# Performance work log

Measured on AMD Instinct MI355X. Metric: run time of the kernel, lower is better.

The kernel has to match this reference:

```python
import jax, jax.numpy as jnp
import numpy as np

B, S, D, H, HD, R = 1, 3072, 2048, 16, 128, 16
ALPHA = 16.0
EPS = 1e-6


def _rope_freqs():
    # standard RoPE angles, interleave-duplicated so freqs[..., 0::2] gives the
    # per-pair cos values exactly as the torch module slices them
    inv = 1.0 / (10000.0 ** (np.arange(0, HD, 2, dtype=np.float32) / HD))  # [HD/2]
    ang = np.arange(S, dtype=np.float32)[:, None] * inv[None, :]           # [S, HD/2]
    cos = np.repeat(np.cos(ang), 2, axis=-1).reshape(1, S, 1, HD)
    sin = np.repeat(np.sin(ang), 2, axis=-1).reshape(1, S, 1, HD)
    return jnp.asarray(cos), jnp.asarray(sin)


def setup_inputs() -> dict:
    key = jax.random.key(0)
    ks = jax.random.split(key, 18)
    n = jax.random.normal
    WS = 0.02  # weight init scale
    freqs_cos, freqs_sin = _rope_freqs()
    return {
        "hidden_states": n(ks[0], (B, S, D), jnp.float32),
        "wq": n(ks[1], (D, D), jnp.float32) * WS,
        "bq": n(ks[2], (D,), jnp.float32) * WS,
        "wk": n(ks[3], (D, D), jnp.float32) * WS,
        "bk": n(ks[4], (D,), jnp.float32) * WS,
        "wv": n(ks[5], (D, D), jnp.float32) * WS,
        "bv": n(ks[6], (D,), jnp.float32) * WS,
        "wo": n(ks[7], (D, D), jnp.float32) * WS,
        "bo": n(ks[8], (D,), jnp.float32) * WS,
        "lq_down": n(ks[9], (R, D), jnp.float32) / R,
        "lq_up": n(ks[10], (D, R), jnp.float32) * WS,
        "lk_down": n(ks[11], (R, D), jnp.float32) / R,
        "lk_up": n(ks[12], (D, R), jnp.float32) * WS,
        "lv_down": n(ks[13], (R, D), jnp.float32) / R,
        "lv_up": n(ks[14], (D, R), jnp.float32) * WS,
        "lo_down": n(ks[15], (R, D), jnp.float32) / R,
        "lo_up": n(ks[16], (D, R), jnp.float32) * WS,
        "norm_q_w": jnp.ones((D,), jnp.float32),
        "norm_k_w": jnp.ones((D,), jnp.float32),
        "freqs_cos": freqs_cos,
        "freqs_sin": freqs_sin,
    }


def _lora(x, w_down, w_up, scale):
    return (x @ w_down.T) @ w_up.T * scale


def _rmsnorm(x, w):
    return x * jax.lax.rsqrt(jnp.mean(x * x, axis=-1, keepdims=True) + EPS) * w


def _apply_rotary(x, freqs_cos, freqs_sin):
    # x: [B,S,H,HD]; freqs: [1,S,1,HD]
    x1, x2 = x[..., 0::2], x[..., 1::2]
    c = freqs_cos[..., 0::2]
    s = freqs_sin[..., 1::2]
    even = x1 * c - x2 * s
    odd = x1 * s + x2 * c
    return jnp.stack([even, odd], axis=-1).reshape(x.shape)


def reference(hidden_states, wq, bq, wk, bk, wv, bv, wo, bo,
              lq_down, lq_up, lk_down, lk_up, lv_down, lv_up, lo_down, lo_up,
              norm_q_w, norm_k_w, freqs_cos, freqs_sin):
    scale = ALPHA / R
    x = hidden_states
    # qkv projections + LoRA adds (self-attention: encoder_hidden_states = hidden_states)
    q = x @ wq.T + bq + _lora(x, lq_down, lq_up, scale)
    k = x @ wk.T + bk + _lora(x, lk_down, lk_up, scale)
    v = x @ wv.T + bv + _lora(x, lv_down, lv_up, scale)
    # RMSNorm over full d_model, then split heads
    q = _rmsnorm(q, norm_q_w).reshape(B, S, H, HD)
    k = _rmsnorm(k, norm_k_w).reshape(B, S, H, HD)
    v = v.reshape(B, S, H, HD)
    # custom strided rotary embedding
    q = _apply_rotary(q, freqs_cos, freqs_sin)
    k = _apply_rotary(k, freqs_cos, freqs_sin)
    # SDPA (non-causal, no mask)
    scores = jnp.einsum('bihd,bjhd->bhij', q, k) / jnp.sqrt(jnp.float32(HD))
    attn = jax.nn.softmax(scores, axis=-1)
    o = jnp.einsum('bhij,bjhd->bihd', attn, v).reshape(B, S, D)
    # output projection + LoRA
    out = o @ wo.T + bo + _lora(o, lo_down, lo_up, scale)
    return out
```

## Files before the change

### kernel.cpp

```cpp
#include <hip/hip_runtime.h>
#include <stdint.h>

#define S_LEN 3072
#define DIM   2048
#define NH    16
#define HDIM  128
#define RANK  16
#define EPS_F 1e-6f
#define LORA_SCALE 1.0f
#define QK_SCALE 0.08838834764831845f
#define SM_MAX 24.0f

typedef unsigned short u16;
typedef __attribute__((ext_vector_type(8))) short short8;
typedef __attribute__((ext_vector_type(4))) float f32x4;
typedef __attribute__((ext_vector_type(4))) unsigned short u16x4;
typedef __attribute__((ext_vector_type(8))) unsigned short u16x8;
typedef __attribute__((ext_vector_type(2))) unsigned short u16x2;
typedef __attribute__((ext_vector_type(4))) float float4a;

__device__ __forceinline__ u16 f2b(float f) {
  uint32_t u = __builtin_bit_cast(uint32_t, f);
  u += 0x7fffu + ((u >> 16) & 1u);
  return (u16)(u >> 16);
}
__device__ __forceinline__ float b2f(u16 b) {
  uint32_t u = ((uint32_t)b) << 16;
  return __builtin_bit_cast(float, u);
}

__device__ __forceinline__ void g2l16(const void* g, void* l) {
  __builtin_amdgcn_global_load_lds(
      (__attribute__((address_space(1))) unsigned int*)g,
      (__attribute__((address_space(3))) unsigned int*)l, 16, 0, 0);
}

__global__ __launch_bounds__(256) void convf2b(const float* __restrict__ in,
                                               u16* __restrict__ out) {
  int i = (blockIdx.x * 256 + threadIdx.x) * 4;
  float4a v = *(const float4a*)(in + i);
  u16x4 o = { f2b(v[0]), f2b(v[1]), f2b(v[2]), f2b(v[3]) };
  *(u16x4*)(out + i) = o;
}

__global__ __launch_bounds__(256) void fold_lora(const float* __restrict__ W,
                                                 const float* __restrict__ lu,
                                                 const float* __restrict__ ld,
                                                 u16* __restrict__ out) {
  __shared__ float lds_ld[16][136];
  __shared__ float lds_lu[64][17];
  const int tid = threadIdx.x;
  const int k0 = blockIdx.x * 128, n0 = blockIdx.y * 64;
  {
    int idx = tid * 8, r = idx >> 7, c = idx & 127;
    const float* src = ld + r * DIM + k0 + c;
#pragma unroll
    for (int e = 0; e < 8; ++e) lds_ld[r][c + e] = src[e];
  }
  {
    int idx = tid * 4, n = idx >> 4, r4 = idx & 15;
    const float* src = lu + (size_t)(n0 + n) * RANK + r4;
#pragma unroll
    for (int e = 0; e < 4; ++e) lds_lu[n][r4 + e] = src[e];
  }
  __syncthreads();
  const int n = tid >> 2;
  const int kg = (tid & 3) * 32;
  float luv[RANK];
#pragma unroll
  for (int r = 0; r < RANK; ++r) luv[r] = lds_lu[n][r];
  const float* wrow = W + (size_t)(n0 + n) * DIM + k0 + kg;
  u16* orow = out + (size_t)(n0 + n) * DIM + k0 + kg;
#pragma unroll
  for (int j = 0; j < 8; ++j) {
    float4a acc = *(const float4a*)(wrow + j * 4);
#pragma unroll
    for (int r = 0; r < RANK; ++r) {
      float4a lv = *(const float4a*)&lds_ld[r][kg + j * 4];
      acc += LORA_SCALE * luv[r] * lv;
    }
    u16x4 o = { f2b(acc[0]), f2b(acc[1]), f2b(acc[2]), f2b(acc[3]) };
    *(u16x4*)(orow + j * 4) = o;
  }
}

__global__ __launch_bounds__(256, 2) void gemm_fused(
    const u16* __restrict__ A, const u16* __restrict__ B,
    const float* __restrict__ b0, const float* __restrict__ b1,
    const float* __restrict__ b2, u16* __restrict__ c0, u16* __restrict__ c1,
    u16* __restrict__ c2, float* __restrict__ Cf) {
  __shared__ __attribute__((aligned(16))) u16 As[128 * 64];
  __shared__ __attribute__((aligned(16))) u16 Bs[128 * 64];
  const int tid = threadIdx.x;
  const int wave = tid >> 6, lane = tid & 63;
  const int quad = lane >> 4, l15 = lane & 15;
  const int m0 = blockIdx.x * 128, n0 = blockIdx.y * 128;
  const int mat = n0 >> 11;
  const float* bias = (mat == 0) ? b0 : (mat == 1 ? b1 : b2);
  u16* Cb = (mat == 0) ? c0 : (mat == 1 ? c1 : c2);
  const int wr = wave >> 1, wc = wave & 1;
  f32x4 acc[4][4] = {};
  for (int kt = 0; kt < DIM / 64; ++kt) {
    __syncthreads();
#pragma unroll
    for (int i = 0; i < 4; ++i) {
      int chunk = i * 256 + wave * 64 + lane;
      int row = chunk >> 3, c8 = chunk & 7;
      g2l16(A + (size_t)(m0 + row) * DIM + kt * 64 + c8 * 8,
            As + (i * 256 + wave * 64) * 8);
      g2l16(B + (size_t)(n0 + row) * DIM + kt * 64 + c8 * 8,
            Bs + (i * 256 + wave * 64) * 8);
    }
    __syncthreads();
#pragma unroll
    for (int kc = 0; kc < 2; ++kc) {
      short8 af[4], bf[4];
#pragma unroll
      for (int tm = 0; tm < 4; ++tm)
        af[tm] = *(const short8*)(As + (wr * 64 + tm * 16 + l15) * 64 +
                                  kc * 32 + quad * 8);
#pragma unroll
      for (int tn = 0; tn < 4; ++tn)
        bf[tn] = *(const short8*)(Bs + (wc * 64 + tn * 16 + l15) * 64 +
                                  kc * 32 + quad * 8);
#pragma unroll
      for (int tm = 0; tm < 4; ++tm)
#pragma unroll
        for (int tn = 0; tn < 4; ++tn)
          acc[tm][tn] = __builtin_amdgcn_mfma_f32_16x16x32_bf16(
              af[tm], bf[tn], acc[tm][tn], 0, 0, 0);
    }
  }
#pragma unroll
  for (int tn = 0; tn < 4; ++tn) {
    int col = n0 + wc * 64 + tn * 16 + l15;
    int colL = col & (DIM - 1);
    float bcol = bias[colL];
#pragma unroll
    for (int tm = 0; tm < 4; ++tm) {
#pragma unroll
      for (int r = 0; r < 4; ++r) {
        int row = m0 + wr * 64 + tm * 16 + quad * 4 + r;
        float val = acc[tm][tn][r] + bcol;
        if (Cf) Cf[(size_t)row * DIM + colL] = val;
        else Cb[(size_t)row * DIM + colL] = f2b(val);
      }
    }
  }
}

__global__ __launch_bounds__(256) void rms_rope(
    u16* __restrict__ q, u16* __restrict__ k,
    const float* __restrict__ nqw, const float* __restrict__ nkw,
    const float* __restrict__ fc, const float* __restrict__ fs) {
  const int s = blockIdx.x, tid = threadIdx.x;
  const int wave = tid >> 6, lane = tid & 63;
  float qv[8], kv[8];
  float sq = 0.f, sk = 0.f;
#pragma unroll
  for (int i = 0; i < 4; ++i) {
    int p = i * 256 + tid;
    u16x2 qa = *(const u16x2*)(q + (size_t)s * DIM + 2 * p);
    u16x2 ka = *(const u16x2*)(k + (size_t)s * DIM + 2 * p);
    qv[2 * i] = b2f(qa[0]); qv[2 * i + 1] = b2f(qa[1]);
    kv[2 * i] = b2f(ka[0]); kv[2 * i + 1] = b2f(ka[1]);
    sq += qv[2 * i] * qv[2 * i] + qv[2 * i + 1] * qv[2 * i + 1];
    sk += kv[2 * i] * kv[2 * i] + kv[2 * i + 1] * kv[2 * i + 1];
  }
#pragma unroll
  for (int off = 32; off > 0; off >>= 1) {
    sq += __shfl_down(sq, off);
    sk += __shfl_down(sk, off);
  }
  __shared__ float part[2][4];
  if (lane == 0) { part[0][wave] = sq; part[1][wave] = sk; }
  __syncthreads();
  float sumq = part[0][0] + part[0][1] + part[0][2] + part[0][3];
  float sumk = part[1][0] + part[1][1] + part[1][2] + part[1][3];
  float rq = rsqrtf(sumq * (1.f / DIM) + EPS_F);
  float rk = rsqrtf(sumk * (1.f / DIM) + EPS_F);
#pragma unroll
  for (int i = 0; i < 4; ++i) {
    int p = i * 256 + tid;
    int ip = p & 63;
    float c = fc[s * HDIM + 2 * ip];
    float sn = fs[s * HDIM + 2 * ip + 1];
    float e = qv[2 * i] * rq * nqw[2 * p];
    float o = qv[2 * i + 1] * rq * nqw[2 * p + 1];
    u16x2 qo = { f2b((e * c - o * sn) * QK_SCALE),
                 f2b((e * sn + o * c) * QK_SCALE) };
    *(u16x2*)(q + (size_t)s * DIM + 2 * p) = qo;
    float e2 = kv[2 * i] * rk * nkw[2 * p];
    float o2 = kv[2 * i + 1] * rk * nkw[2 * p + 1];
    u16x2 ko = { f2b(e2 * c - o2 * sn), f2b(e2 * sn + o2 * c) };
    *(u16x2*)(k + (size_t)s * DIM + 2 * p) = ko;
  }
}

__global__ __launch_bounds__(256) void transpose_v(const u16* __restrict__ in,
                                                   u16* __restrict__ out) {
  __shared__ float tile[64][65];
  const int bs = blockIdx.x * 64;
  const int bd = blockIdx.y * 64;
  const int tid = threadIdx.x;
#pragma unroll
  for (int i = 0; i < 4; ++i) {
    int idx = i * 1024 + tid * 4;
    int r = idx >> 6, c = idx & 63;
    u16x4 v = *(const u16x4*)(in + (size_t)(bs + r) * DIM + bd + c);
    tile[r][c + 0] = b2f(v[0]); tile[r][c + 1] = b2f(v[1]);
    tile[r][c + 2] = b2f(v[2]); tile[r][c + 3] = b2f(v[3]);
  }
  __syncthreads();
#pragma unroll
  for (int i = 0; i < 2; ++i) {
    int cid = i * 256 + tid;
    int dr = cid >> 3, sc = cid & 7;
    u16x8 o;
#pragma unroll
    for (int e = 0; e < 8; ++e) o[e] = f2b(tile[sc * 8 + e][dr]);
    *(u16x8*)(out + (size_t)(bd + dr) * S_LEN + bs + sc * 8) = o;
  }
}

__global__ __launch_bounds__(128, 2) void flash_attn(
    const u16* __restrict__ qb, const u16* __restrict__ kb,
    const u16* __restrict__ vt, u16* __restrict__ ob) {
  __shared__ __attribute__((aligned(16))) u16 Ks[64 * 128];
  __shared__ __attribute__((aligned(16))) u16 Vt[144 * 64];
  __shared__ __attribute__((aligned(16))) u16 Ps[4][16 * 64];
  const int tid = threadIdx.x;
  const int wave = tid >> 6, lane = tid & 63;
  const int quad = lane >> 4, l15 = lane & 15;
  const int q0 = blockIdx.x * 64, h = blockIdx.y;
  short8 qf[2][4];
#pragma unroll
  for (int t = 0; t < 2; ++t) {
    int qrow = q0 + wave * 32 + t * 16 + l15;
#pragma unroll
    for (int kc = 0; kc < 4; ++kc)
      qf[t][kc] = *(const short8*)(qb + (size_t)qrow * DIM + h * HDIM +
                                   kc * 32 + quad * 8);
  }
  {
    int idx = tid * 8, d = 128 + (idx >> 6), c = idx & 63;
    u16 fill = (d == 128) ? (u16)0x3F80 : (u16)0;
    u16x8 v = { fill, fill, fill, fill, fill, fill, fill, fill };
    *(u16x8*)(Vt + d * 64 + c) = v;
  }
  f32x4 of[2][9] = {};
  for (int it = 0; it < S_LEN / 64; ++it) {
    const int j0 = it * 64;
    __syncthreads();
#pragma unroll
    for (int i = 0; i < 8; ++i) {
      int slot = i * 128 + tid;
      {
        int j = slot >> 4, csp = slot & 15;
        int cg = csp ^ (j & 7);
        g2l16(kb + (size_t)(j0 + j) * DIM + h * HDIM + cg * 8,
              Ks + (i * 128 + wave * 64) * 8);
      }
      {
        int d = slot >> 3, cbp = slot & 7;
        int cbg = cbp ^ (d & 7);
        g2l16(vt + (size_t)(h * HDIM + d) * S_LEN + j0 + cbg * 8,
              Vt + (i * 128 + wave * 64) * 8);
      }
    }
    __syncthreads();
    f32x4 sf[2][4] = {};
#pragma unroll
    for (int kc = 0; kc < 4; ++kc) {
#pragma unroll
      for (int tn = 0; tn < 4; ++tn) {
        int j = tn * 16 + l15;
        int csp = (kc * 4 + quad) ^ (j & 7);
        short8 bfr = *(const short8*)(Ks + j * 128 + csp * 8);
        sf[0][tn] = __builtin_amdgcn_mfma_f32_16x16x32_bf16(qf[0][kc], bfr,
                                                            sf[0][tn], 0, 0, 0);
        sf[1][tn] = __builtin_amdgcn_mfma_f32_16x16x32_bf16(qf[1][kc], bfr,
                                                            sf[1][tn], 0, 0, 0);
      }
    }
#pragma unroll
    for (int t = 0; t < 2; ++t) {
      u16* pw = &Ps[wave * 2 + t][0];
#pragma unroll
      for (int r = 0; r < 4; ++r) {
        int row = quad * 4 + r;
#pragma unroll
        for (int tn = 0; tn < 4; ++tn) {
          float p = __expf(sf[t][tn][r] - SM_MAX);
          int cb = (tn * 2 + (l15 >> 3)) ^ (row & 7);
          pw[row * 64 + cb * 8 + (l15 & 7)] = f2b(p);
        }
      }
    }
    __syncthreads();
#pragma unroll
    for (int kc2 = 0; kc2 < 2; ++kc2) {
      short8 af0 = *(const short8*)(&Ps[wave * 2 + 0][0] + l15 * 64 +
                                    (((kc2 * 4 + quad) ^ (l15 & 7)) * 8));
      short8 af1 = *(const short8*)(&Ps[wave * 2 + 1][0] + l15 * 64 +
                                    (((kc2 * 4 + quad) ^ (l15 & 7)) * 8));
#pragma unroll
      for (int dt = 0; dt < 9; ++dt) {
        int d = dt * 16 + l15;
        int cb = (kc2 * 4 + quad) ^ (d & 7);
        short8 bfr = *(const short8*)(Vt + d * 64 + cb * 8);
        of[0][dt] = __builtin_amdgcn_mfma_f32_16x16x32_bf16(af0, bfr,
                                                            of[0][dt], 0, 0, 0);
        of[1][dt] = __builtin_amdgcn_mfma_f32_16x16x32_bf16(af1, bfr,
                                                            of[1][dt], 0, 0, 0);
      }
    }
  }
#pragma unroll
  for (int t = 0; t < 2; ++t) {
#pragma unroll
    for (int r = 0; r < 4; ++r) {
      float li = __shfl(of[t][8][r], lane & 48);
      float inv = 1.f / li;
      int row = q0 + wave * 32 + t * 16 + quad * 4 + r;
#pragma unroll
      for (int dt = 0; dt < 8; ++dt)
        ob[(size_t)row * DIM + h * HDIM + dt * 16 + l15] =
            f2b(of[t][dt][r] * inv);
    }
  }
}

extern "C" void kernel_launch(void* const* d_in, const int* in_sizes, int n_in,
                              void* d_out, int out_size, void* d_ws,
                              size_t ws_size, hipStream_t stream) {
  (void)in_sizes; (void)n_in; (void)out_size; (void)ws_size;
  const float* x   = (const float*)d_in[0];
  const float* wq  = (const float*)d_in[1];
  const float* bq  = (const float*)d_in[2];
  const float* wk  = (const float*)d_in[3];
  const float* bk  = (const float*)d_in[4];
  const float* wv  = (const float*)d_in[5];
  const float* bv  = (const float*)d_in[6];
  const float* wo  = (const float*)d_in[7];
  const float* bo  = (const float*)d_in[8];
  const float* lqd = (const float*)d_in[9];
  const float* lqu = (const float*)d_in[10];
  const float* lkd = (const float*)d_in[11];
  const float* lku = (const float*)d_in[12];
  const float* lvd = (const float*)d_in[13];
  const float* lvu = (const float*)d_in[14];
  const float* lod = (const float*)d_in[15];
  const float* lou = (const float*)d_in[16];
  const float* nqw = (const float*)d_in[17];
  const float* nkw = (const float*)d_in[18];
  const float* fc  = (const float*)d_in[19];
  const float* fs  = (const float*)d_in[20];

  char* ws = (char*)d_ws;
  size_t off = 0;
  auto alloc = [&](size_t bytes) {
    void* p = ws + off;
    off += (bytes + 255) & ~(size_t)255;
    return p;
  };
  const size_t SD2 = (size_t)S_LEN * DIM * 2;
  const size_t WW  = (size_t)DIM * DIM;
  u16* xb    = (u16*)alloc(SD2);
  u16* wqkvb = (u16*)alloc(3 * WW * 2);
  u16* wob   = (u16*)alloc(WW * 2);
  u16* q16   = (u16*)alloc(SD2);
  u16* k16   = (u16*)alloc(SD2);
  u16* v16   = (u16*)alloc(SD2);
  u16* vbT   = (u16*)alloc(SD2);
  u16* ob    = (u16*)alloc(SD2);

  dim3 foldg(DIM / 128, DIM / 64);
  convf2b<<<S_LEN * DIM / 1024, 256, 0, stream>>>(x, xb);
  fold_lora<<<foldg, 256, 0, stream>>>(wq, lqu, lqd, wqkvb);
  fold_lora<<<foldg, 256, 0, stream>>>(wk, lku, lkd, wqkvb + WW);
  fold_lora<<<foldg, 256, 0, stream>>>(wv, lvu, lvd, wqkvb + 2 * WW);
  fold_lora<<<foldg, 256, 0, stream>>>(wo, lou, lod, wob);
  gemm_fused<<<dim3(S_LEN / 128, 3 * DIM / 128), 256, 0, stream>>>(
      xb, wqkvb, bq, bk, bv, q16, k16, v16, nullptr);
  rms_rope<<<S_LEN, 256, 0, stream>>>(q16, k16, nqw, nkw, fc, fs);
  transpose_v<<<dim3(S_LEN / 64, DIM / 64), 256, 0, stream>>>(v16, vbT);
  flash_attn<<<dim3(S_LEN / 64, NH), 128, 0, stream>>>(q16, k16, vbT, ob);
  gemm_fused<<<dim3(S_LEN / 128, DIM / 128), 256, 0, stream>>>(
      ob, wob, bo, nullptr, nullptr, nullptr, nullptr, nullptr, (float*)d_out);
}
```

Before: 481.0 us.

## Retile attention, templatize GEMM tile height, vectorize rms_rope loads

Flash attention now uses 256-thread blocks covering 192 query rows, 48 per wave, so each K/V tile loaded into LDS serves more queries. The grid shrinks to 16x16 blocks. The GEMM becomes a template on M-tile height with launch bounds of 3 waves, and the output projection uses 64-row tiles to double its block count. rms_rope switches to 8-wide vector loads and stores, and the P matrix uses truncating bf16 conversion instead of rounding. The trade-offs are fewer attention blocks (256) for the CU count, more registers per wave, and a slight precision change in P.

```diff
diff --git a/kernel.cpp b/kernel.cpp
--- a/kernel.cpp
+++ b/kernel.cpp
@@ -23,6 +23,9 @@
   uint32_t u = __builtin_bit_cast(uint32_t, f);
   u += 0x7fffu + ((u >> 16) & 1u);
   return (u16)(u >> 16);
+}
+__device__ __forceinline__ u16 f2b_trunc(float f) {
+  return (u16)(__builtin_bit_cast(uint32_t, f) >> 16);
 }
 __device__ __forceinline__ float b2f(u16 b) {
   uint32_t u = ((uint32_t)b) << 16;
@@ -84,47 +87,54 @@
   }
 }
 
-__global__ __launch_bounds__(256, 2) void gemm_fused(
+template <int TM>
+__global__ __launch_bounds__(256, 3) void gemm_core(
     const u16* __restrict__ A, const u16* __restrict__ B,
     const float* __restrict__ b0, const float* __restrict__ b1,
     const float* __restrict__ b2, u16* __restrict__ c0, u16* __restrict__ c1,
     u16* __restrict__ c2, float* __restrict__ Cf) {
-  __shared__ __attribute__((aligned(16))) u16 As[128 * 64];
+  constexpr int WM = TM * 16, BM = 2 * WM;
+  __shared__ __attribute__((aligned(16))) u16 As[BM * 64];
   __shared__ __attribute__((aligned(16))) u16 Bs[128 * 64];
   const int tid = threadIdx.x;
   const int wave = tid >> 6, lane = tid & 63;
   const int quad = lane >> 4, l15 = lane & 15;
-  const int m0 = blockIdx.x * 128, n0 = blockIdx.y * 128;
+  const int m0 = blockIdx.x * BM, n0 = blockIdx.y * 128;
   const int mat = n0 >> 11;
   const float* bias = (mat == 0) ? b0 : (mat == 1 ? b1 : b2);
   u16* Cb = (mat == 0) ? c0 : (mat == 1 ? c1 : c2);
   const int wr = wave >> 1, wc = wave & 1;
-  f32x4 acc[4][4] = {};
+  f32x4 acc[TM][4] = {};
   for (int kt = 0; kt < DIM / 64; ++kt) {
     __syncthreads();
 #pragma unroll
-    for (int i = 0; i < 4; ++i) {
-      int chunk = i * 256 + wave * 64 + lane;
+    for (int i = 0; i < TM * 2; ++i) {
+      int chunk = i * 256 + tid;
       int row = chunk >> 3, c8 = chunk & 7;
       g2l16(A + (size_t)(m0 + row) * DIM + kt * 64 + c8 * 8,
             As + (i * 256 + wave * 64) * 8);
+    }
+#pragma unroll
+    for (int i = 0; i < 4; ++i) {
+      int chunk = i * 256 + tid;
+      int row = chunk >> 3, c8 = chunk & 7;
       g2l16(B + (size_t)(n0 + row) * DIM + kt * 64 + c8 * 8,
             Bs + (i * 256 + wave * 64) * 8);
     }
     __syncthreads();
 #pragma unroll
     for (int kc = 0; kc < 2; ++kc) {
-      short8 af[4], bf[4];
-#pragma unroll
-      for (int tm = 0; tm < 4; ++tm)
-        af[tm] = *(const short8*)(As + (wr * 64 + tm * 16 + l15) * 64 +
+      short8 af[TM], bf[4];
+#pragma unroll
+      for (int tm = 0; tm < TM; ++tm)
+        af[tm] = *(const short8*)(As + (wr * WM + tm * 16 + l15) * 64 +
                                   kc * 32 + quad * 8);
 #pragma unroll
       for (int tn = 0; tn < 4; ++tn)
         bf[tn] = *(const short8*)(Bs + (wc * 64 + tn * 16 + l15) * 64 +
                                   kc * 32 + quad * 8);
 #pragma unroll
-      for (int tm = 0; tm < 4; ++tm)
+      for (int tm = 0; tm < TM; ++tm)
 #pragma unroll
         for (int tn = 0; tn < 4; ++tn)
           acc[tm][tn] = __builtin_amdgcn_mfma_f32_16x16x32_bf16(
@@ -137,10 +147,10 @@
     int colL = col & (DIM - 1);
     float bcol = bias[colL];
 #pragma unroll
-    for (int tm = 0; tm < 4; ++tm) {
+    for (int tm = 0; tm < TM; ++tm) {
 #pragma unroll
       for (int r = 0; r < 4; ++r) {
-        int row = m0 + wr * 64 + tm * 16 + quad * 4 + r;
+        int row = m0 + wr * WM + tm * 16 + quad * 4 + r;
         float val = acc[tm][tn][r] + bcol;
         if (Cf) Cf[(size_t)row * DIM + colL] = val;
         else Cb[(size_t)row * DIM + colL] = f2b(val);
@@ -155,17 +165,16 @@
     const float* __restrict__ fc, const float* __restrict__ fs) {
   const int s = blockIdx.x, tid = threadIdx.x;
   const int wave = tid >> 6, lane = tid & 63;
+  const int e0 = tid * 8;
+  u16x8 qa = *(const u16x8*)(q + (size_t)s * DIM + e0);
+  u16x8 ka = *(const u16x8*)(k + (size_t)s * DIM + e0);
   float qv[8], kv[8];
   float sq = 0.f, sk = 0.f;
 #pragma unroll
-  for (int i = 0; i < 4; ++i) {
-    int p = i * 256 + tid;
-    u16x2 qa = *(const u16x2*)(q + (size_t)s * DIM + 2 * p);
-    u16x2 ka = *(const u16x2*)(k + (size_t)s * DIM + 2 * p);
-    qv[2 * i] = b2f(qa[0]); qv[2 * i + 1] = b2f(qa[1]);
-    kv[2 * i] = b2f(ka[0]); kv[2 * i + 1] = b2f(ka[1]);
-    sq += qv[2 * i] * qv[2 * i] + qv[2 * i + 1] * qv[2 * i + 1];
-    sk += kv[2 * i] * kv[2 * i] + kv[2 * i + 1] * kv[2 * i + 1];
+  for (int i = 0; i < 8; ++i) {
+    qv[i] = b2f(qa[i]); kv[i] = b2f(ka[i]);
+    sq += qv[i] * qv[i];
+    sk += kv[i] * kv[i];
   }
 #pragma unroll
   for (int off = 32; off > 0; off >>= 1) {
@@ -179,22 +188,34 @@
   float sumk = part[1][0] + part[1][1] + part[1][2] + part[1][3];
   float rq = rsqrtf(sumq * (1.f / DIM) + EPS_F);
   float rk = rsqrtf(sumk * (1.f / DIM) + EPS_F);
-#pragma unroll
-  for (int i = 0; i < 4; ++i) {
-    int p = i * 256 + tid;
-    int ip = p & 63;
-    float c = fc[s * HDIM + 2 * ip];
-    float sn = fs[s * HDIM + 2 * ip + 1];
-    float e = qv[2 * i] * rq * nqw[2 * p];
-    float o = qv[2 * i + 1] * rq * nqw[2 * p + 1];
-    u16x2 qo = { f2b((e * c - o * sn) * QK_SCALE),
-                 f2b((e * sn + o * c) * QK_SCALE) };
-    *(u16x2*)(q + (size_t)s * DIM + 2 * p) = qo;
-    float e2 = kv[2 * i] * rk * nkw[2 * p];
-    float o2 = kv[2 * i + 1] * rk * nkw[2 * p + 1];
-    u16x2 ko = { f2b(e2 * c - o2 * sn), f2b(e2 * sn + o2 * c) };
-    *(u16x2*)(k + (size_t)s * DIM + 2 * p) = ko;
-  }
+  const int fb = e0 & 127;
+  float4a fc0 = *(const float4a*)(fc + s * HDIM + fb);
+  float4a fc1 = *(const float4a*)(fc + s * HDIM + fb + 4);
+  float4a fs0 = *(const float4a*)(fs + s * HDIM + fb);
+  float4a fs1 = *(const float4a*)(fs + s * HDIM + fb + 4);
+  float4a nq0 = *(const float4a*)(nqw + e0);
+  float4a nq1 = *(const float4a*)(nqw + e0 + 4);
+  float4a nk0 = *(const float4a*)(nkw + e0);
+  float4a nk1 = *(const float4a*)(nkw + e0 + 4);
+  float cj[4] = { fc0[0], fc0[2], fc1[0], fc1[2] };
+  float sj[4] = { fs0[1], fs0[3], fs1[1], fs1[3] };
+  float nq[8] = { nq0[0], nq0[1], nq0[2], nq0[3], nq1[0], nq1[1], nq1[2], nq1[3] };
+  float nk[8] = { nk0[0], nk0[1], nk0[2], nk0[3], nk1[0], nk1[1], nk1[2], nk1[3] };
+  u16x8 qo, ko;
+#pragma unroll
+  for (int j = 0; j < 4; ++j) {
+    float c = cj[j], sn = sj[j];
+    float e = qv[2 * j] * rq * nq[2 * j];
+    float o = qv[2 * j + 1] * rq * nq[2 * j + 1];
+    qo[2 * j]     = f2b((e * c - o * sn) * QK_SCALE);
+    qo[2 * j + 1] = f2b((e * sn + o * c) * QK_SCALE);
+    float e2 = kv[2 * j] * rk * nk[2 * j];
+    float o2 = kv[2 * j + 1] * rk * nk[2 * j + 1];
+    ko[2 * j]     = f2b(e2 * c - o2 * sn);
+    ko[2 * j + 1] = f2b(e2 * sn + o2 * c);
+  }
+  *(u16x8*)(q + (size_t)s * DIM + e0) = qo;
+  *(u16x8*)(k + (size_t)s * DIM + e0) = ko;
 }
 
 __global__ __launch_bounds__(256) void transpose_v(const u16* __restrict__ in,
@@ -223,53 +244,53 @@
   }
 }
 
-__global__ __launch_bounds__(128, 2) void flash_attn(
+__global__ __launch_bounds__(256, 1) void flash_attn(
     const u16* __restrict__ qb, const u16* __restrict__ kb,
     const u16* __restrict__ vt, u16* __restrict__ ob) {
   __shared__ __attribute__((aligned(16))) u16 Ks[64 * 128];
   __shared__ __attribute__((aligned(16))) u16 Vt[144 * 64];
-  __shared__ __attribute__((aligned(16))) u16 Ps[4][16 * 64];
+  __shared__ __attribute__((aligned(16))) u16 Ps[4][3][16 * 64];
   const int tid = threadIdx.x;
   const int wave = tid >> 6, lane = tid & 63;
   const int quad = lane >> 4, l15 = lane & 15;
-  const int q0 = blockIdx.x * 64, h = blockIdx.y;
-  short8 qf[2][4];
-#pragma unroll
-  for (int t = 0; t < 2; ++t) {
-    int qrow = q0 + wave * 32 + t * 16 + l15;
+  const int q0 = blockIdx.x * 192, h = blockIdx.y;
+  short8 qf[3][4];
+#pragma unroll
+  for (int t = 0; t < 3; ++t) {
+    int qrow = q0 + wave * 48 + t * 16 + l15;
 #pragma unroll
     for (int kc = 0; kc < 4; ++kc)
       qf[t][kc] = *(const short8*)(qb + (size_t)qrow * DIM + h * HDIM +
                                    kc * 32 + quad * 8);
   }
   {
-    int idx = tid * 8, d = 128 + (idx >> 6), c = idx & 63;
+    int idx = tid * 4, d = 128 + (idx >> 6), c = idx & 63;
     u16 fill = (d == 128) ? (u16)0x3F80 : (u16)0;
-    u16x8 v = { fill, fill, fill, fill, fill, fill, fill, fill };
-    *(u16x8*)(Vt + d * 64 + c) = v;
-  }
-  f32x4 of[2][9] = {};
+    u16x4 v = { fill, fill, fill, fill };
+    *(u16x4*)(Vt + d * 64 + c) = v;
+  }
+  f32x4 of[3][9] = {};
   for (int it = 0; it < S_LEN / 64; ++it) {
     const int j0 = it * 64;
     __syncthreads();
 #pragma unroll
-    for (int i = 0; i < 8; ++i) {
-      int slot = i * 128 + tid;
-      {
-        int j = slot >> 4, csp = slot & 15;
-        int cg = csp ^ (j & 7);
-        g2l16(kb + (size_t)(j0 + j) * DIM + h * HDIM + cg * 8,
-              Ks + (i * 128 + wave * 64) * 8);
-      }
-      {
-        int d = slot >> 3, cbp = slot & 7;
-        int cbg = cbp ^ (d & 7);
-        g2l16(vt + (size_t)(h * HDIM + d) * S_LEN + j0 + cbg * 8,
-              Vt + (i * 128 + wave * 64) * 8);
-      }
+    for (int i = 0; i < 4; ++i) {
+      int slot = i * 256 + tid;
+      int j = slot >> 4, csp = slot & 15;
+      int cg = csp ^ (j & 7);
+      g2l16(kb + (size_t)(j0 + j) * DIM + h * HDIM + cg * 8,
+            Ks + (i * 256 + wave * 64) * 8);
+    }
+#pragma unroll
+    for (int i = 0; i < 4; ++i) {
+      int slot = i * 256 + tid;
+      int d = slot >> 3, cbp = slot & 7;
+      int cbg = cbp ^ (d & 7);
+      g2l16(vt + (size_t)(h * HDIM + d) * S_LEN + j0 + cbg * 8,
+            Vt + (i * 256 + wave * 64) * 8);
     }
     __syncthreads();
-    f32x4 sf[2][4] = {};
+    f32x4 sf[3][4] = {};
 #pragma unroll
     for (int kc = 0; kc < 4; ++kc) {
 #pragma unroll
@@ -277,15 +298,15 @@
         int j = tn * 16 + l15;
         int csp = (kc * 4 + quad) ^ (j & 7);
         short8 bfr = *(const short8*)(Ks + j * 128 + csp * 8);
-        sf[0][tn] = __builtin_amdgcn_mfma_f32_16x16x32_bf16(qf[0][kc], bfr,
-                                                            sf[0][tn], 0, 0, 0);
-        sf[1][tn] = __builtin_amdgcn_mfma_f32_16x16x32_bf16(qf[1][kc], bfr,
-                                                            sf[1][tn], 0, 0, 0);
+#pragma unroll
+        for (int t = 0; t < 3; ++t)
+          sf[t][tn] = __builtin_amdgcn_mfma_f32_16x16x32_bf16(
+              qf[t][kc], bfr, sf[t][tn], 0, 0, 0);
       }
     }
 #pragma unroll
-    for (int t = 0; t < 2; ++t) {
-      u16* pw = &Ps[wave * 2 + t][0];
+    for (int t = 0; t < 3; ++t) {
+      u16* pw = &Ps[wave][t][0];
 #pragma unroll
       for (int r = 0; r < 4; ++r) {
         int row = quad * 4 + r;
@@ -293,36 +314,37 @@
         for (int tn = 0; tn < 4; ++tn) {
           float p = __expf(sf[t][tn][r] - SM_MAX);
           int cb = (tn * 2 + (l15 >> 3)) ^ (row & 7);
-          pw[row * 64 + cb * 8 + (l15 & 7)] = f2b(p);
+          pw[row * 64 + cb * 8 + (l15 & 7)] = f2b_trunc(p);
         }
       }
     }
     __syncthreads();
 #pragma unroll
     for (int kc2 = 0; kc2 < 2; ++kc2) {
-      short8 af0 = *(const short8*)(&Ps[wave * 2 + 0][0] + l15 * 64 +
-                                    (((kc2 * 4 + quad) ^ (l15 & 7)) * 8));
-      short8 af1 = *(const short8*)(&Ps[wave * 2 + 1][0] + l15 * 64 +
-                                    (((kc2 * 4 + quad) ^ (l15 & 7)) * 8));
+      short8 af[3];
+#pragma unroll
+      for (int t = 0; t < 3; ++t)
+        af[t] = *(const short8*)(&Ps[wave][t][0] + l15 * 64 +
+                                 (((kc2 * 4 + quad) ^ (l15 & 7)) * 8));
 #pragma unroll
       for (int dt = 0; dt < 9; ++dt) {
         int d = dt * 16 + l15;
         int cb = (kc2 * 4 + quad) ^ (d & 7);
         short8 bfr = *(const short8*)(Vt + d * 64 + cb * 8);
-        of[0][dt] = __builtin_amdgcn_mfma_f32_16x16x32_bf16(af0, bfr,
-                                                            of[0][dt], 0, 0, 0);
-        of[1][dt] = __builtin_amdgcn_mfma_f32_16x16x32_bf16(af1, bfr,
-                                                            of[1][dt], 0, 0, 0);
+#pragma unroll
+        for (int t = 0; t < 3; ++t)
+          of[t][dt] = __builtin_amdgcn_mfma_f32_16x16x32_bf16(
+              af[t], bfr, of[t][dt], 0, 0, 0);
       }
     }
   }
 #pragma unroll
-  for (int t = 0; t < 2; ++t) {
+  for (int t = 0; t < 3; ++t) {
 #pragma unroll
     for (int r = 0; r < 4; ++r) {
       float li = __shfl(of[t][8][r], lane & 48);
       float inv = 1.f / li;
-      int row = q0 + wave * 32 + t * 16 + quad * 4 + r;
+      int row = q0 + wave * 48 + t * 16 + quad * 4 + r;
 #pragma unroll
       for (int dt = 0; dt < 8; ++dt)
         ob[(size_t)row * DIM + h * HDIM + dt * 16 + l15] =
@@ -381,11 +403,11 @@
   fold_lora<<<foldg, 256, 0, stream>>>(wk, lku, lkd, wqkvb + WW);
   fold_lora<<<foldg, 256, 0, stream>>>(wv, lvu, lvd, wqkvb + 2 * WW);
   fold_lora<<<foldg, 256, 0, stream>>>(wo, lou, lod, wob);
-  gemm_fused<<<dim3(S_LEN / 128, 3 * DIM / 128), 256, 0, stream>>>(
+  gemm_core<4><<<dim3(S_LEN / 128, 3 * DIM / 128), 256, 0, stream>>>(
       xb, wqkvb, bq, bk, bv, q16, k16, v16, nullptr);
   rms_rope<<<S_LEN, 256, 0, stream>>>(q16, k16, nqw, nkw, fc, fs);
   transpose_v<<<dim3(S_LEN / 64, DIM / 64), 256, 0, stream>>>(v16, vbT);
-  flash_attn<<<dim3(S_LEN / 64, NH), 128, 0, stream>>>(q16, k16, vbT, ob);
-  gemm_fused<<<dim3(S_LEN / 128, DIM / 128), 256, 0, stream>>>(
+  flash_attn<<<dim3(S_LEN / 192, NH), 256, 0, stream>>>(q16, k16, vbT, ob);
+  gemm_core<2><<<dim3(S_LEN / 64, DIM / 128), 256, 0, stream>>>(
       ob, wob, bo, nullptr, nullptr, nullptr, nullptr, nullptr, (float*)d_out);
 }
```

After: 501.3 us. +4.2%, slower.
